# Performance work log

Hardware: AMD Instinct MI355X
Metric: run time of the kernel (lower is better)

Reference implementation:

```python
import jax, jax.numpy as jnp
import numpy as np

B = 4             # graphs per batch
POS_RANGE = 240.0 # pos lives in [0, 240)^3
VOXELS = (20.0, 30.0, 50.0, 80.0)
NEG = -1e30


def _basis(u):
    # open B-spline basis, degree 1, kernel_size 2, dim 3 -> 8 weights per edge
    cols = []
    for k in range(8):
        w = (u[:, 0] if k & 4 else 1.0 - u[:, 0])
        w = w * (u[:, 1] if k & 2 else 1.0 - u[:, 1])
        w = w * (u[:, 2] if k & 1 else 1.0 - u[:, 2])
        cols.append(w)
    return jnp.stack(cols, axis=1)  # [E, 8]


def _cartesian(pos, src, dst, emask):
    # T.Cartesian(cat=False, norm=True): rel pos scaled into [0,1]
    rel = pos[src] - pos[dst]
    m = jnp.max(jnp.where(emask[:, None], jnp.abs(rel), 0.0))
    return rel / (2.0 * jnp.maximum(m, 1e-9)) + 0.5


def _spline_conv(x, src, dst, pseudo, emask, W, Wr, b, n_nodes):
    # out_i = mean_{j->i} sum_k B_k(u_ij) x_j W_k + x_i Wr + b
    basis = _basis(pseudo) * emask[:, None].astype(x.dtype)  # [E,8]
    xk = jnp.einsum('ni,kio->nko', x, W)                     # [N,8,O]
    msg = basis[:, 0, None] * xk[src, 0]
    for k in range(1, 8):
        msg = msg + basis[:, k, None] * xk[src, k]           # [E,O]
    agg = jax.ops.segment_sum(msg, dst, num_segments=n_nodes)
    deg = jax.ops.segment_sum(emask.astype(x.dtype), dst, num_segments=n_nodes)
    return agg / jnp.maximum(deg, 1.0)[:, None] + x @ Wr + b


def _voxel_ids(pos, batch, vs):
    G = int(np.ceil(POS_RANGE / vs))
    c = jnp.clip(jnp.floor(pos / vs).astype(jnp.int64), 0, G - 1)
    cell = (c[:, 0] * G + c[:, 1]) * G + c[:, 2]
    return batch * (G ** 3) + cell, G ** 3


def _max_pool(x, pos, batch, valid, src, dst, emask, vs):
    # voxel-grid max pooling: nodes become fixed voxel cells (empty cells masked)
    nid, ncells = _voxel_ids(pos, batch, vs)
    n_new = B * ncells
    xm = jnp.where(valid[:, None], x, NEG)
    x_p = jax.ops.segment_max(xm, nid, num_segments=n_new)
    cnt = jax.ops.segment_sum(valid.astype(x.dtype), nid, num_segments=n_new)
    v_new = cnt > 0
    x_p = jnp.where(v_new[:, None], x_p, 0.0)
    pos_p = jax.ops.segment_sum(pos * valid[:, None].astype(pos.dtype), nid, num_segments=n_new)
    pos_p = pos_p / jnp.maximum(cnt, 1.0)[:, None]
    batch_p = jnp.arange(n_new, dtype=jnp.int64) // ncells
    # coarsen edges: remap to cells, drop self loops, coalesce at fixed size
    s2, d2 = nid[src], nid[dst]
    sent = n_new * n_new
    key = jnp.where(emask & (s2 != d2), s2 * n_new + d2, sent)
    uk = jnp.unique(key, size=key.shape[0], fill_value=sent)
    em = uk != sent
    uk = jnp.where(em, uk, 0)
    return x_p, pos_p, batch_p, v_new, uk // n_new, uk % n_new, em


def setup_inputs():
    key = jax.random.key(0)
    ks = jax.random.split(key, 24)
    NP, DEG = 5000, 8
    N = B * NP
    E = N * DEG
    x = jax.random.normal(ks[0], (N, 1), dtype=jnp.float32)
    pos = jax.random.uniform(ks[1], (N, 3), dtype=jnp.float32) * POS_RANGE
    src = jnp.repeat(jnp.arange(N, dtype=jnp.int64), DEG)
    delta = jax.random.randint(ks[2], (E,), 1, 100, dtype=jnp.int64)
    dst = (src // NP) * NP + (src % NP + delta) % NP   # intra-graph edges
    edge_index = jnp.stack([src, dst])
    batch = jnp.arange(N, dtype=jnp.int64) // NP
    sizes = [1, 64, 128, 256, 512]
    params = {}
    for l in range(4):
        ci, co = sizes[l], sizes[l + 1]
        params[f'W{l+1}'] = jax.random.normal(ks[3 + 3 * l], (8, ci, co), dtype=jnp.float32) / np.sqrt(8.0 * ci)
        params[f'Wr{l+1}'] = jax.random.normal(ks[4 + 3 * l], (ci, co), dtype=jnp.float32) / np.sqrt(float(ci))
        params[f'b{l+1}'] = jnp.zeros((co,), dtype=jnp.float32)
    params['fc1_w'] = jax.random.normal(ks[16], (64 * 512, 1024), dtype=jnp.float32) / np.sqrt(64.0 * 512.0)
    params['fc1_b'] = jnp.zeros((1024,), dtype=jnp.float32)
    params['fc2_w'] = jax.random.normal(ks[17], (1024, 1), dtype=jnp.float32) / np.sqrt(1024.0)
    params['fc2_b'] = jnp.zeros((1,), dtype=jnp.float32)
    return dict(x=x, pos=pos, edge_index=edge_index, batch=batch, **params)


def reference(x, pos, edge_index, batch, W1, Wr1, b1, W2, Wr2, b2, W3, Wr3, b3,
              W4, Wr4, b4, fc1_w, fc1_b, fc2_w, fc2_b):
    src, dst = edge_index[0], edge_index[1]
    n_nodes = x.shape[0]
    valid = jnp.ones((n_nodes,), dtype=bool)
    emask = jnp.ones((src.shape[0],), dtype=bool)
    Ws = [(W1, Wr1, b1), (W2, Wr2, b2), (W3, Wr3, b3), (W4, Wr4, b4)]
    for l in range(4):
        pseudo = _cartesian(pos, src, dst, emask)
        W, Wr, b = Ws[l]
        x = jax.nn.elu(_spline_conv(x, src, dst, pseudo, emask, W, Wr, b, n_nodes))
        if l < 3:
            x, pos, batch, valid, src, dst, emask = _max_pool(x, pos, batch, valid, src, dst, emask, VOXELS[l])
            n_nodes = x.shape[0]
    # MaxPoolingX(voxel=80, size=64): ceil(240/80)^3 = 27 <= 64 slots per graph
    nid, ncells = _voxel_ids(pos, batch, VOXELS[3])
    cluster = batch * 64 + (nid % ncells)
    xm = jnp.where(valid[:, None], x, NEG)
    xg = jax.ops.segment_max(xm, cluster, num_segments=B * 64)
    xg = jnp.where(xg <= NEG / 2, 0.0, xg)      # empty slots -> 0 (scatter-max default)
    xg = xg.reshape(B, 64 * 512)
    h = jax.nn.elu(xg @ fc1_w + fc1_b)           # dropout = identity (eval mode)
    return jax.nn.elu(h @ fc2_w + fc2_b)         # [B, 1]
```

## Files before the change

kernel.cpp:

```cpp
#include <hip/hip_runtime.h>

static constexpr int E0 = 160000;
static constexpr int NL0 = 20000;
static constexpr int NL1 = 6912;
static constexpr int NL2 = 2048;
static constexpr int NL3 = 500;

typedef short bf16x8 __attribute__((ext_vector_type(8)));
typedef float f32x4 __attribute__((ext_vector_type(4)));

__device__ __forceinline__ unsigned f2ord(float f) {
  unsigned u = __float_as_uint(f);
  return (u & 0x80000000u) ? ~u : (u | 0x80000000u);
}
__device__ __forceinline__ float ord2f(unsigned u) {
  unsigned v = (u & 0x80000000u) ? (u & 0x7fffffffu) : ~u;
  return __uint_as_float(v);
}
__device__ __forceinline__ float eluf(float x) { return x > 0.f ? x : expm1f(x); }
__device__ __forceinline__ void basis8(float u0, float u1, float u2, float* w) {
  float a0 = 1.f - u0, a1 = 1.f - u1, a2 = 1.f - u2;
  w[0] = a0*a1*a2; w[1] = a0*a1*u2; w[2] = a0*u1*a2; w[3] = a0*u1*u2;
  w[4] = u0*a1*a2; w[5] = u0*a1*u2; w[6] = u0*u1*a2; w[7] = u0*u1*u2;
}
__device__ __forceinline__ unsigned short f2b(float f) {
  unsigned u = __float_as_uint(f);
  return (unsigned short)((u + 0x7fffu + ((u >> 16) & 1u)) >> 16);
}
__device__ __forceinline__ float b2f(unsigned short h) {
  return __uint_as_float(((unsigned)h) << 16);
}
__device__ __forceinline__ int clampi(int v, int lo, int hi) {
  return v < lo ? lo : (v > hi ? hi : v);
}

__device__ __forceinline__ void mfma_tile(const unsigned short* __restrict__ Ah,
    const unsigned short* __restrict__ Al, const unsigned short* __restrict__ Bh,
    const unsigned short* __restrict__ Bl, int M, long K, int m0, int n0,
    int kbeg, int ksl, char* smem, f32x4* acc) {
  auto Ash = (unsigned short (*)[40])(smem);
  auto Asl = (unsigned short (*)[40])(smem + 5120);
  auto Bsh = (unsigned short (*)[40])(smem + 10240);
  auto Bsl = (unsigned short (*)[40])(smem + 15360);
  int t = threadIdx.x;
  int r = t >> 2, sg = (t & 3) * 8;
  int w = t >> 6, lane = t & 63;
  int ar = (w << 4) + (lane & 15), kq = (lane >> 4) << 3;
  for (int kt = 0; kt < ksl; kt += 32) {
    bf16x8 va = {}, vl = {};
    if (m0 + r < M) {
      long ga = (long)(m0 + r) * K + kbeg + kt + sg;
      va = *(const bf16x8*)&Ah[ga];
      vl = *(const bf16x8*)&Al[ga];
    }
    *(bf16x8*)&Ash[r][sg] = va;
    *(bf16x8*)&Asl[r][sg] = vl;
    long gb = (long)(n0 + r) * K + kbeg + kt + sg;
    *(bf16x8*)&Bsh[r][sg] = *(const bf16x8*)&Bh[gb];
    *(bf16x8*)&Bsl[r][sg] = *(const bf16x8*)&Bl[gb];
    __syncthreads();
    bf16x8 ah = *(const bf16x8*)&Ash[ar][kq];
    bf16x8 al = *(const bf16x8*)&Asl[ar][kq];
    #pragma unroll
    for (int nt = 0; nt < 4; nt++) {
      int br = (nt << 4) + (lane & 15);
      bf16x8 bh = *(const bf16x8*)&Bsh[br][kq];
      bf16x8 bl = *(const bf16x8*)&Bsl[br][kq];
      acc[nt] = __builtin_amdgcn_mfma_f32_16x16x32_bf16(al, bh, acc[nt], 0, 0, 0);
      acc[nt] = __builtin_amdgcn_mfma_f32_16x16x32_bf16(ah, bl, acc[nt], 0, 0, 0);
      acc[nt] = __builtin_amdgcn_mfma_f32_16x16x32_bf16(ah, bh, acc[nt], 0, 0, 0);
    }
    __syncthreads();
  }
}

__global__ __launch_bounds__(256)
void k_prep(const int* __restrict__ src0, const int* __restrict__ dst0,
            const float* __restrict__ pos0, const float* __restrict__ x0,
            int* __restrict__ degi, int4* __restrict__ erec0u, float* __restrict__ mbuf,
            const float* __restrict__ W1, const float* __restrict__ Wr1, float* __restrict__ wc1,
            const float* __restrict__ W2, const float* __restrict__ Wr2,
            const float* __restrict__ W3, const float* __restrict__ Wr3,
            const float* __restrict__ W4, const float* __restrict__ Wr4,
            unsigned short* __restrict__ w2h, unsigned short* __restrict__ w2l,
            unsigned short* __restrict__ w3h, unsigned short* __restrict__ w3l,
            unsigned short* __restrict__ w4h, unsigned short* __restrict__ w4l) {
  __shared__ __align__(16) float T[64][65];
  __shared__ float red[4];
  int tid = blockIdx.x * 256 + threadIdx.x, gsz = gridDim.x * 256;
  float v = 0.f;
  for (int e = tid; e < E0; e += gsz) {
    int s = src0[e], d = dst0[e];
    atomicAdd(&degi[d], 1);
    float r0 = pos0[s*3]   - pos0[d*3];
    float r1 = pos0[s*3+1] - pos0[d*3+1];
    float r2 = pos0[s*3+2] - pos0[d*3+2];
    erec0u[e] = make_int4(__float_as_int(x0[s]), __float_as_int(r0),
                          __float_as_int(r1), __float_as_int(r2));
    v = fmaxf(v, fmaxf(fabsf(r0), fmaxf(fabsf(r1), fabsf(r2))));
  }
  #pragma unroll
  for (int off = 32; off; off >>= 1) v = fmaxf(v, __shfl_down(v, off, 64));
  if ((threadIdx.x & 63) == 0) red[threadIdx.x >> 6] = v;
  __syncthreads();
  if (threadIdx.x == 0)
    atomicMax((unsigned*)mbuf,
              __float_as_uint(fmaxf(fmaxf(red[0], red[1]), fmaxf(red[2], red[3]))));
  for (int b = blockIdx.x; b < 378; b += gridDim.x) {
    const float *W, *Wr; unsigned short *oh, *ol; int K, N, kt, nt;
    if (b < 18)      { W = W2; Wr = Wr2; oh = w2h; ol = w2l; K = 576;  N = 128; kt = b / 2; nt = b % 2; }
    else if (b < 90) { int q = b - 18; W = W3; Wr = Wr3; oh = w3h; ol = w3l; K = 1152; N = 256; kt = q / 4; nt = q % 4; }
    else             { int q = b - 90; W = W4; Wr = Wr4; oh = w4h; ol = w4l; K = 2304; N = 512; kt = q / 8; nt = q % 8; }
    int k0 = kt * 64, n0 = nt * 64, KW = K - K / 9;
    __syncthreads();
    for (int i = threadIdx.x; i < 4096; i += 256) {
      int kk = i >> 6, nn = i & 63, k = k0 + kk;
      T[kk][nn] = (k < KW) ? W[(long)k * N + n0 + nn] : Wr[(long)(k - KW) * N + n0 + nn];
    }
    __syncthreads();
    for (int i = threadIdx.x; i < 4096; i += 256) {
      int nn = i >> 6, kk = i & 63;
      float vv = T[kk][nn];
      unsigned short hu = f2b(vv), lu = f2b(vv - b2f(hu));
      long o = (long)(n0 + nn) * K + k0 + kk;
      oh[o] = hu; ol[o] = lu;
    }
  }
  if (blockIdx.x == 0)
    for (int i = threadIdx.x; i < 576; i += 256)
      wc1[i] = (i < 512) ? W1[i] : Wr1[i - 512];
}

__global__ void k_alloc(int* __restrict__ degi, int* __restrict__ rowbeg,
                        int* __restrict__ rowlen, int* __restrict__ cursor,
                        int* __restrict__ ctr, int N) {
  int n = blockIdx.x * 256 + threadIdx.x;
  if (n >= N) return;
  int len = degi[n];
  int st = atomicAdd(ctr, len);
  rowbeg[n] = st; cursor[n] = st; rowlen[n] = len; degi[n] = 0;
}

__global__ void k_scat(const int4* __restrict__ eu, const int* __restrict__ du,
                       const int* __restrict__ ecnt, int ecap,
                       int* __restrict__ cursor, int4* __restrict__ es) {
  int n = ecnt ? *ecnt : ecap;
  for (int e = blockIdx.x * 256 + threadIdx.x; e < n; e += gridDim.x * 256) {
    int p = atomicAdd(&cursor[du[e]], 1);
    es[p] = eu[e];
  }
}

__global__ __launch_bounds__(256)
void k_l1(const float* __restrict__ pos0, const float* __restrict__ x0,
          const int4* __restrict__ erec, const int* __restrict__ rowbeg,
          const int* __restrict__ rowlen, const float* __restrict__ mbuf,
          const float* __restrict__ wc1, const float* __restrict__ b1,
          unsigned* __restrict__ pord1, float* __restrict__ cnt1,
          float* __restrict__ possum1, int* __restrict__ nid) {
  __shared__ float ys9[256][12];
  int t = threadIdx.x;
  int d = blockIdx.x * 256 + t;
  float inv = 0.5f / fmaxf(mbuf[0], 1e-9f);
  if (d < NL0) {
    int beg = rowbeg[d], len = rowlen[d];
    float acc[8] = {};
    for (int j = beg; j < beg + len; j++) {
      int4 rc = erec[j];
      float xv = __int_as_float(rc.x);
      float u0 = __int_as_float(rc.y) * inv + 0.5f;
      float u1 = __int_as_float(rc.z) * inv + 0.5f;
      float u2 = __int_as_float(rc.w) * inv + 0.5f;
      float w[8]; basis8(u0, u1, u2, w);
      #pragma unroll
      for (int k = 0; k < 8; k++) acc[k] += w[k] * xv;
    }
    float sc = 1.f / fmaxf((float)len, 1.f);
    #pragma unroll
    for (int k = 0; k < 8; k++) ys9[t][k] = acc[k] * sc;
    ys9[t][8]  = x0[d];
    ys9[t][9]  = pos0[d*3];
    ys9[t][10] = pos0[d*3+1];
    ys9[t][11] = pos0[d*3+2];
  }
  __syncthreads();
  int lane = t & 63, wv = t >> 6;
  float wcol[9];
  #pragma unroll
  for (int k = 0; k < 8; k++) wcol[k] = wc1[k * 64 + lane];
  wcol[8] = wc1[512 + lane];
  float bb = b1[lane];
  int base = blockIdx.x * 256 + wv * 64;
  for (int i = 0; i < 64; i++) {
    int dd = base + i;
    if (dd >= NL0) break;
    int li = wv * 64 + i;
    float v = bb + ys9[li][8] * wcol[8];
    #pragma unroll
    for (int k = 0; k < 8; k++) v += ys9[li][k] * wcol[k];
    v = eluf(v);
    float pd0 = ys9[li][9], pd1 = ys9[li][10], pd2 = ys9[li][11];
    int c0 = clampi((int)floorf(pd0 / 20.f), 0, 11);
    int c1 = clampi((int)floorf(pd1 / 20.f), 0, 11);
    int c2 = clampi((int)floorf(pd2 / 20.f), 0, 11);
    int id = (dd / 5000) * 1728 + (c0 * 12 + c1) * 12 + c2;
    atomicMax(&pord1[(long)id * 64 + lane], f2ord(v));
    if (lane == 0) {
      nid[dd] = id;
      atomicAdd(&cnt1[id], 1.f);
      atomicAdd(&possum1[id*3],   pd0);
      atomicAdd(&possum1[id*3+1], pd1);
      atomicAdd(&possum1[id*3+2], pd2);
    }
  }
}

__global__ __launch_bounds__(256)
void k_pedge(const int4* __restrict__ erecf, const int* __restrict__ srcf,
             const int* __restrict__ dstf, const int* __restrict__ ecntf, int ecap,
             const int* __restrict__ nid, int Nn, unsigned* __restrict__ bitmap,
             int4* __restrict__ erecu, int* __restrict__ dstu, int* __restrict__ ecntc,
             int* __restrict__ degi, const float* __restrict__ possum,
             const float* __restrict__ cnt, float* __restrict__ mo) {
  __shared__ float red[4];
  int n = ecntf ? *ecntf : ecap;
  int lane = threadIdx.x & 63;
  int stride = gridDim.x * 256;
  float vmax = 0.f;
  for (int base = blockIdx.x * 256; base < n; base += stride) {
    int e = base + threadIdx.x;
    bool win = false;
    int s2 = 0, d2 = 0;
    float r0 = 0.f, r1 = 0.f, r2 = 0.f;
    if (e < n) {
      int sL = erecf ? erecf[e].x : srcf[e];
      int dL = dstf[e];
      s2 = nid[sL]; d2 = nid[dL];
      if (s2 != d2) {
        float ics = 1.f / fmaxf(cnt[s2], 1.f), icd = 1.f / fmaxf(cnt[d2], 1.f);
        r0 = possum[s2*3]   * ics - possum[d2*3]   * icd;
        r1 = possum[s2*3+1] * ics - possum[d2*3+1] * icd;
        r2 = possum[s2*3+2] * ics - possum[d2*3+2] * icd;
        vmax = fmaxf(vmax, fmaxf(fabsf(r0), fmaxf(fabsf(r1), fabsf(r2))));
        unsigned key = (unsigned)s2 * (unsigned)Nn + (unsigned)d2;
        unsigned bit = 1u << (key & 31);
        unsigned old = atomicOr(&bitmap[key >> 5], bit);
        win = !(old & bit);
      }
    }
    unsigned long long mask = __ballot(win);
    if (mask) {
      int leader = __ffsll((unsigned long long)mask) - 1;
      int bq = 0;
      if (lane == leader) bq = atomicAdd(ecntc, __popcll(mask));
      bq = __shfl(bq, leader, 64);
      if (win) {
        int q = bq + __popcll(mask & ((1ULL << lane) - 1ULL));
        erecu[q] = make_int4(s2, __float_as_int(r0), __float_as_int(r1), __float_as_int(r2));
        dstu[q] = d2;
        atomicAdd(&degi[d2], 1);
      }
    }
  }
  #pragma unroll
  for (int off = 32; off; off >>= 1) vmax = fmaxf(vmax, __shfl_down(vmax, off, 64));
  if ((threadIdx.x & 63) == 0) red[threadIdx.x >> 6] = vmax;
  __syncthreads();
  if (threadIdx.x == 0)
    atomicMax((unsigned*)mo,
              __float_as_uint(fmaxf(fmaxf(red[0], red[1]), fmaxf(red[2], red[3]))));
}

template<int ES>
__global__ __launch_bounds__(256)
void k_gather(const unsigned* __restrict__ pordc, const int4* __restrict__ erec,
              const int* __restrict__ rowbeg, const int* __restrict__ rowlen,
              const float* __restrict__ mbuf,
              unsigned short* __restrict__ ysh, unsigned short* __restrict__ ysl,
              int N, int Ci, int nchunk) {
  __shared__ float comb[4][64][8];
  int wv = threadIdx.x >> 6, lane = threadIdx.x & 63;
  int gw = blockIdx.x * 4 + wv;
  int job = gw / ES, sub = gw % ES;
  int d = job / nchunk, ch = job % nchunk;
  bool active = d < N;
  float inv = 0.5f / fmaxf(mbuf[0], 1e-9f);
  int co = ch * 64 + lane;
  float acc[8] = {};
  int beg = 0, len = 0;
  if (active) {
    beg = rowbeg[d]; len = rowlen[d];
    int end = beg + len;
    int j = beg + sub;
    for (; j + 3 * ES < end; j += 4 * ES) {
      int4 ra = erec[j], rb = erec[j + ES], rc = erec[j + 2 * ES], rd = erec[j + 3 * ES];
      float xa = ord2f(pordc[(long)ra.x * Ci + co]);
      float xb = ord2f(pordc[(long)rb.x * Ci + co]);
      float xc = ord2f(pordc[(long)rc.x * Ci + co]);
      float xd = ord2f(pordc[(long)rd.x * Ci + co]);
      float wa[8], wb[8], wc[8], wd[8];
      basis8(__int_as_float(ra.y) * inv + 0.5f, __int_as_float(ra.z) * inv + 0.5f,
             __int_as_float(ra.w) * inv + 0.5f, wa);
      basis8(__int_as_float(rb.y) * inv + 0.5f, __int_as_float(rb.z) * inv + 0.5f,
             __int_as_float(rb.w) * inv + 0.5f, wb);
      basis8(__int_as_float(rc.y) * inv + 0.5f, __int_as_float(rc.z) * inv + 0.5f,
             __int_as_float(rc.w) * inv + 0.5f, wc);
      basis8(__int_as_float(rd.y) * inv + 0.5f, __int_as_float(rd.z) * inv + 0.5f,
             __int_as_float(rd.w) * inv + 0.5f, wd);
      #pragma unroll
      for (int k = 0; k < 8; k++)
        acc[k] += wa[k] * xa + wb[k] * xb + wc[k] * xc + wd[k] * xd;
    }
    for (; j < end; j += ES) {
      int4 ra = erec[j];
      float xa = ord2f(pordc[(long)ra.x * Ci + co]);
      float wa[8];
      basis8(__int_as_float(ra.y) * inv + 0.5f, __int_as_float(ra.z) * inv + 0.5f,
             __int_as_float(ra.w) * inv + 0.5f, wa);
      #pragma unroll
      for (int k = 0; k < 8; k++) acc[k] += wa[k] * xa;
    }
  }
  if (ES > 1) {
    #pragma unroll
    for (int k = 0; k < 8; k++) comb[wv][lane][k] = acc[k];
    __syncthreads();
    if (sub != 0 || !active) return;
    #pragma unroll
    for (int s = 1; s < ES; s++)
      #pragma unroll
      for (int k = 0; k < 8; k++) acc[k] += comb[wv + s][lane][k];
  } else if (!active) return;
  float sc = 1.f / fmaxf((float)len, 1.f);
  long row = (long)d * 9 * Ci;
  #pragma unroll
  for (int k = 0; k < 8; k++) {
    float v = acc[k] * sc;
    unsigned short hu = f2b(v);
    ysh[row + k * Ci + co] = hu;
    ysl[row + k * Ci + co] = f2b(v - b2f(hu));
  }
  unsigned od = pordc[(long)d * Ci + co];
  float xdv = (od == 0u) ? 0.f : ord2f(od);
  unsigned short hu = f2b(xdv);
  ysh[row + 8 * Ci + co] = hu;
  ysl[row + 8 * Ci + co] = f2b(xdv - b2f(hu));
}

__global__ __launch_bounds__(256)
void k_gemmpool(const unsigned short* __restrict__ ysh, const unsigned short* __restrict__ ysl,
                const unsigned short* __restrict__ Bh, const unsigned short* __restrict__ Bl,
                int M, int N, int K, const float* __restrict__ bias,
                const float* __restrict__ possum, const float* __restrict__ cnt,
                int div, float vs, int G, int NC,
                unsigned* __restrict__ pordn, float* __restrict__ cntn,
                float* __restrict__ possumn, int* __restrict__ nid) {
  __shared__ __align__(16) char smem[20480];
  int nbx = N >> 6;
  int bx = blockIdx.x % nbx, by = blockIdx.x / nbx;
  int m0 = by * 64, n0 = bx * 64;
  f32x4 acc[4] = {};
  mfma_tile(ysh, ysl, Bh, Bl, M, K, m0, n0, 0, K, smem, acc);
  int w = threadIdx.x >> 6, lane = threadIdx.x & 63;
  int row0 = m0 + (w << 4) + ((lane >> 4) << 2);
  int colb = n0 + (lane & 15);
  #pragma unroll
  for (int q = 0; q < 4; q++) {
    int gm = row0 + q;
    float c = cnt[gm];
    float ic = 1.f / fmaxf(c, 1.f);
    float p0 = possum[gm*3] * ic, p1 = possum[gm*3+1] * ic, p2 = possum[gm*3+2] * ic;
    int c0 = clampi((int)floorf(p0 / vs), 0, G - 1);
    int c1 = clampi((int)floorf(p1 / vs), 0, G - 1);
    int c2 = clampi((int)floorf(p2 / vs), 0, G - 1);
    int id = (gm / div) * NC + (c0 * G + c1) * G + c2;
    bool vl = c > 0.f;
    if (bx == 0 && (lane & 15) == 0) {
      nid[gm] = id;
      if (vl) {
        atomicAdd(&cntn[id], 1.f);
        atomicAdd(&possumn[id*3],   p0);
        atomicAdd(&possumn[id*3+1], p1);
        atomicAdd(&possumn[id*3+2], p2);
      }
    }
    if (vl) {
      #pragma unroll
      for (int nt = 0; nt < 4; nt++) {
        int col = colb + nt * 16;
        float v = eluf(acc[nt][q] + bias[col]);
        atomicMax(&pordn[(long)id * N + col], f2ord(v));
      }
    }
  }
}

__global__ __launch_bounds__(256)
void k_gemm4(const unsigned short* __restrict__ ysh, const unsigned short* __restrict__ ysl,
             const unsigned short* __restrict__ Bh, const unsigned short* __restrict__ Bl,
             float* __restrict__ Cp) {
  __shared__ __align__(16) char smem[20480];
  int z = blockIdx.x >> 6, rem = blockIdx.x & 63, bx = rem & 7, by = rem >> 3;
  int m0 = by * 64, n0 = bx * 64;
  f32x4 acc[4] = {};
  mfma_tile(ysh, ysl, Bh, Bl, 500, 2304, m0, n0, z * 576, 576, smem, acc);
  float* Co = Cp + (long)z * 256000;
  int w = threadIdx.x >> 6, lane = threadIdx.x & 63;
  int row0 = m0 + (w << 4) + ((lane >> 4) << 2);
  int colb = n0 + (lane & 15);
  #pragma unroll
  for (int nt = 0; nt < 4; nt++)
    #pragma unroll
    for (int q = 0; q < 4; q++) {
      int gm = row0 + q;
      if (gm < 500) Co[(long)gm * 512 + colb + nt * 16] = acc[nt][q];
    }
}

__global__ void k_reduce4(const float* __restrict__ Cp, const float* __restrict__ b4,
                          const float* __restrict__ possum3, const float* __restrict__ cnt3,
                          unsigned* __restrict__ xg) {
  int idx = blockIdx.x * 256 + threadIdx.x;
  if (idx >= 256000) return;
  int n = idx >> 9, o = idx & 511;
  float s = Cp[idx] + Cp[idx + 256000] + Cp[idx + 512000] + Cp[idx + 768000];
  float v = eluf(s + b4[o]);
  float c = cnt3[n];
  if (c <= 0.f) return;
  float ic = 1.f / c;
  float p0 = possum3[n*3] * ic, p1 = possum3[n*3+1] * ic, p2 = possum3[n*3+2] * ic;
  int c0 = clampi((int)floorf(p0 / 80.f), 0, 2);
  int c1 = clampi((int)floorf(p1 / 80.f), 0, 2);
  int c2 = clampi((int)floorf(p2 / 80.f), 0, 2);
  int cl = (n / 125) * 64 + (c0 * 3 + c1) * 3 + c2;
  atomicMax(&xg[(long)cl * 512 + o], f2ord(v));
}

__global__ __launch_bounds__(128)
void k_fc1(const unsigned* __restrict__ xg_ord, const float* __restrict__ w,
           float* __restrict__ h) {
  int cellhalf = blockIdx.x >> 3, jb = blockIdx.x & 7;
  int cell = cellhalf >> 1, half = cellhalf & 1;
  int j = jb * 128 + threadIdx.x;
  __shared__ float xs[4][256];
  for (int q = threadIdx.x; q < 1024; q += 128) {
    int b = q >> 8, ci = q & 255;
    unsigned o = xg_ord[((b * 64 + cell) << 9) + half * 256 + ci];
    xs[b][ci] = (o == 0u) ? 0.f : ord2f(o);
  }
  __syncthreads();
  float a0 = 0, a1 = 0, a2 = 0, a3 = 0;
  int cbase = cell * 512 + half * 256;
  for (int ci = 0; ci < 256; ci++) {
    float ww = w[(long)(cbase + ci) * 1024 + j];
    a0 += xs[0][ci] * ww; a1 += xs[1][ci] * ww;
    a2 += xs[2][ci] * ww; a3 += xs[3][ci] * ww;
  }
  atomicAdd(&h[j], a0);        atomicAdd(&h[1024 + j], a1);
  atomicAdd(&h[2048 + j], a2); atomicAdd(&h[3072 + j], a3);
}

__global__ void k_fc2(const float* __restrict__ h, const float* __restrict__ fb1,
                      const float* __restrict__ w, const float* __restrict__ b,
                      float* __restrict__ out) {
  int bb = blockIdx.x, t = threadIdx.x;
  float a = 0;
  for (int j = t; j < 1024; j += 256) a += eluf(h[bb * 1024 + j] + fb1[j]) * w[j];
  for (int off = 32; off; off >>= 1) a += __shfl_down(a, off, 64);
  __shared__ float red[4];
  int lane = t & 63, wv = t >> 6;
  if (lane == 0) red[wv] = a;
  __syncthreads();
  if (t == 0) out[bb] = eluf(red[0] + red[1] + red[2] + red[3] + b[0]);
}

extern "C" void kernel_launch(void* const* d_in, const int* in_sizes, int n_in,
                              void* d_out, int out_size, void* d_ws, size_t ws_size,
                              hipStream_t stream) {
  const float* x0   = (const float*)d_in[0];
  const float* pos0 = (const float*)d_in[1];
  const int*   ei   = (const int*)d_in[2];
  const float* W1 = (const float*)d_in[4],  *Wr1 = (const float*)d_in[5],  *b1 = (const float*)d_in[6];
  const float* W2 = (const float*)d_in[7],  *Wr2 = (const float*)d_in[8],  *b2 = (const float*)d_in[9];
  const float* W3 = (const float*)d_in[10], *Wr3 = (const float*)d_in[11], *b3 = (const float*)d_in[12];
  const float* W4 = (const float*)d_in[13], *Wr4 = (const float*)d_in[14], *b4 = (const float*)d_in[15];
  const float* fw1 = (const float*)d_in[16], *fb1 = (const float*)d_in[17];
  const float* fw2 = (const float*)d_in[18], *fb2 = (const float*)d_in[19];
  float* out = (float*)d_out;
  const int* src0 = ei;
  const int* dst0 = ei + E0;

  char* ws = (char*)d_ws;
  size_t off = 0;
  auto alloc = [&](size_t bytes) -> void* {
    off = (off + 255) & ~(size_t)255;
    void* q = ws + off; off += bytes; return q;
  };
  int4* erec0u = (int4*)alloc((size_t)E0 * 16);
  int4* erec_s = (int4*)alloc((size_t)E0 * 16);
  int4* eu_a   = (int4*)alloc((size_t)E0 * 16);
  int4* eu_b   = (int4*)alloc((size_t)E0 * 16);
  int* du_a = (int*)alloc(E0 * 4);
  int* du_b = (int*)alloc(E0 * 4);
  int* nid  = (int*)alloc(NL0 * 4);
  int* rowbeg = (int*)alloc(NL0 * 4);
  int* rowlen = (int*)alloc(NL0 * 4);
  int* cursor = (int*)alloc(NL0 * 4);
  unsigned short* ysh = (unsigned short*)alloc((size_t)NL1 * 576 * 2);
  unsigned short* ysl = (unsigned short*)alloc((size_t)NL1 * 576 * 2);
  float* wc1 = (float*)alloc(576 * 4);
  unsigned short* w2h = (unsigned short*)alloc((size_t)576 * 128 * 2);
  unsigned short* w2l = (unsigned short*)alloc((size_t)576 * 128 * 2);
  unsigned short* w3h = (unsigned short*)alloc((size_t)1152 * 256 * 2);
  unsigned short* w3l = (unsigned short*)alloc((size_t)1152 * 256 * 2);
  unsigned short* w4h = (unsigned short*)alloc((size_t)2304 * 512 * 2);
  unsigned short* w4l = (unsigned short*)alloc((size_t)2304 * 512 * 2);
  float* Cp = (float*)alloc((size_t)4 * 256000 * 4);
  char* z0 = (char*)alloc(0);
  unsigned* pord1 = (unsigned*)alloc((size_t)NL1 * 64 * 4);
  unsigned* pord2 = (unsigned*)alloc((size_t)NL2 * 128 * 4);
  unsigned* pord3 = (unsigned*)alloc((size_t)NL3 * 256 * 4);
  unsigned* xg    = (unsigned*)alloc((size_t)4 * 64 * 512 * 4);
  float* cnt1 = (float*)alloc(NL1 * 4);
  float* cnt2 = (float*)alloc(NL2 * 4);
  float* cnt3 = (float*)alloc(NL3 * 4);
  float* possum1 = (float*)alloc(NL1 * 12);
  float* possum2 = (float*)alloc(NL2 * 12);
  float* possum3 = (float*)alloc(NL3 * 12);
  size_t bm1w = ((size_t)NL1 * NL1 + 31) / 32;
  size_t bm2w = ((size_t)NL2 * NL2 + 31) / 32;
  size_t bm3w = ((size_t)NL3 * NL3 + 31) / 32;
  unsigned* bm1 = (unsigned*)alloc(bm1w * 4);
  unsigned* bm2 = (unsigned*)alloc(bm2w * 4);
  unsigned* bm3 = (unsigned*)alloc(bm3w * 4);
  int* degi = (int*)alloc(NL0 * 4);
  float* mbuf = (float*)alloc(64);
  int* ecnt = (int*)(mbuf + 8);
  int* ctr  = (int*)(mbuf + 12);
  float* h = (float*)alloc(4096 * 4);
  char* zend = (char*)alloc(0);
  size_t zbytes = (size_t)(zend - z0);
  (void)ws_size; (void)in_sizes; (void)n_in; (void)out_size;

  auto cdiv = [](long a, long b) { return (int)((a + b - 1) / b); };

  hipMemsetAsync(z0, 0, zbytes, stream);

  k_prep<<<512, 256, 0, stream>>>(src0, dst0, pos0, x0, degi, erec0u, mbuf,
                                  W1, Wr1, wc1, W2, Wr2, W3, Wr3, W4, Wr4,
                                  w2h, w2l, w3h, w3l, w4h, w4l);
  k_alloc<<<cdiv(NL0, 256), 256, 0, stream>>>(degi, rowbeg, rowlen, cursor, ctr + 0, NL0);
  k_scat<<<512, 256, 0, stream>>>(erec0u, dst0, nullptr, E0, cursor, erec_s);
  k_l1<<<cdiv(NL0, 256), 256, 0, stream>>>(pos0, x0, erec_s, rowbeg, rowlen, mbuf,
                                           wc1, b1, pord1, cnt1, possum1, nid);
  k_pedge<<<512, 256, 0, stream>>>(nullptr, src0, dst0, nullptr, E0, nid, NL1, bm1,
                                   eu_a, du_a, ecnt + 0, degi, possum1, cnt1, mbuf + 1);
  k_alloc<<<cdiv(NL1, 256), 256, 0, stream>>>(degi, rowbeg, rowlen, cursor, ctr + 1, NL1);
  k_scat<<<512, 256, 0, stream>>>(eu_a, du_a, ecnt + 0, E0, cursor, erec_s);
  k_gather<1><<<cdiv(NL1, 4), 256, 0, stream>>>(pord1, erec_s, rowbeg, rowlen, mbuf + 1,
                                                ysh, ysl, NL1, 64, 1);
  k_gemmpool<<<(128 / 64) * (NL1 / 64), 256, 0, stream>>>(
      ysh, ysl, w2h, w2l, NL1, 128, 576, b2, possum1, cnt1,
      1728, 30.f, 8, 512, pord2, cnt2, possum2, nid);
  k_pedge<<<512, 256, 0, stream>>>(eu_a, nullptr, du_a, ecnt + 0, E0, nid, NL2, bm2,
                                   eu_b, du_b, ecnt + 1, degi, possum2, cnt2, mbuf + 2);
  k_alloc<<<cdiv(NL2, 256), 256, 0, stream>>>(degi, rowbeg, rowlen, cursor, ctr + 2, NL2);
  k_scat<<<512, 256, 0, stream>>>(eu_b, du_b, ecnt + 1, E0, cursor, erec_s);
  k_gather<2><<<cdiv(NL2 * 2 * 2, 4), 256, 0, stream>>>(pord2, erec_s, rowbeg, rowlen, mbuf + 2,
                                                        ysh, ysl, NL2, 128, 2);
  k_gemmpool<<<(256 / 64) * (NL2 / 64), 256, 0, stream>>>(
      ysh, ysl, w3h, w3l, NL2, 256, 1152, b3, possum2, cnt2,
      512, 50.f, 5, 125, pord3, cnt3, possum3, nid);
  k_pedge<<<512, 256, 0, stream>>>(eu_b, nullptr, du_b, ecnt + 1, E0, nid, NL3, bm3,
                                   eu_a, du_a, ecnt + 2, degi, possum3, cnt3, mbuf + 3);
  k_alloc<<<cdiv(NL3, 256), 256, 0, stream>>>(degi, rowbeg, rowlen, cursor, ctr + 3, NL3);
  k_scat<<<512, 256, 0, stream>>>(eu_a, du_a, ecnt + 2, E0, cursor, erec_s);
  k_gather<4><<<cdiv(NL3 * 4 * 4, 4), 256, 0, stream>>>(pord3, erec_s, rowbeg, rowlen, mbuf + 3,
                                                        ysh, ysl, NL3, 256, 4);
  k_gemm4<<<256, 256, 0, stream>>>(ysh, ysl, w4h, w4l, Cp);
  k_reduce4<<<cdiv(256000, 256), 256, 0, stream>>>(Cp, b4, possum3, cnt3, xg);
  k_fc1<<<27 * 2 * 8, 128, 0, stream>>>(xg, fw1, h);
  k_fc2<<<4, 256, 0, stream>>>(h, fb1, fw2, fb2, out);
}
```

Before: 413.1 us.

## Split layer-1 conv into edge-parallel aggregation and per-node pooling kernels

The fused layer-1 kernel is split in two. The first kernel assigns 8 threads per destination node to walk its edge list, reduces the 8 basis accumulators with xor shuffles, and writes them to a global scratch buffer. The second kernel gives each node its own wavefront to do the small matvec, ELU and voxel atomics. Before, one thread walked each node's whole edge list and one wave serially looped over 64 nodes for the pooling atomics, so the goal is more parallelism and less serial latency. The cost is an extra launch and a global round trip through the scratch buffer.

```diff
diff --git a/kernel.cpp b/kernel.cpp
--- a/kernel.cpp
+++ b/kernel.cpp
@@ -152,66 +152,69 @@
 }
 
 __global__ __launch_bounds__(256)
-void k_l1(const float* __restrict__ pos0, const float* __restrict__ x0,
-          const int4* __restrict__ erec, const int* __restrict__ rowbeg,
-          const int* __restrict__ rowlen, const float* __restrict__ mbuf,
-          const float* __restrict__ wc1, const float* __restrict__ b1,
-          unsigned* __restrict__ pord1, float* __restrict__ cnt1,
-          float* __restrict__ possum1, int* __restrict__ nid) {
-  __shared__ float ys9[256][12];
+void k_l1a(const int4* __restrict__ erec, const int* __restrict__ rowbeg,
+           const int* __restrict__ rowlen, const float* __restrict__ mbuf,
+           float* __restrict__ ysg) {
   int t = threadIdx.x;
-  int d = blockIdx.x * 256 + t;
+  int d = blockIdx.x * 32 + (t >> 3);
+  if (d >= NL0) return;
+  int sub = t & 7;
   float inv = 0.5f / fmaxf(mbuf[0], 1e-9f);
-  if (d < NL0) {
-    int beg = rowbeg[d], len = rowlen[d];
-    float acc[8] = {};
-    for (int j = beg; j < beg + len; j++) {
-      int4 rc = erec[j];
-      float xv = __int_as_float(rc.x);
-      float u0 = __int_as_float(rc.y) * inv + 0.5f;
-      float u1 = __int_as_float(rc.z) * inv + 0.5f;
-      float u2 = __int_as_float(rc.w) * inv + 0.5f;
-      float w[8]; basis8(u0, u1, u2, w);
-      #pragma unroll
-      for (int k = 0; k < 8; k++) acc[k] += w[k] * xv;
-    }
+  int beg = rowbeg[d], len = rowlen[d], end = beg + len;
+  float acc[8] = {};
+  for (int j = beg + sub; j < end; j += 8) {
+    int4 rc = erec[j];
+    float xv = __int_as_float(rc.x);
+    float w[8];
+    basis8(__int_as_float(rc.y) * inv + 0.5f, __int_as_float(rc.z) * inv + 0.5f,
+           __int_as_float(rc.w) * inv + 0.5f, w);
+    #pragma unroll
+    for (int k = 0; k < 8; k++) acc[k] += w[k] * xv;
+  }
+  #pragma unroll
+  for (int m = 1; m < 8; m <<= 1)
+    #pragma unroll
+    for (int k = 0; k < 8; k++) acc[k] += __shfl_xor(acc[k], m, 64);
+  if (sub == 0) {
     float sc = 1.f / fmaxf((float)len, 1.f);
-    #pragma unroll
-    for (int k = 0; k < 8; k++) ys9[t][k] = acc[k] * sc;
-    ys9[t][8]  = x0[d];
-    ys9[t][9]  = pos0[d*3];
-    ys9[t][10] = pos0[d*3+1];
-    ys9[t][11] = pos0[d*3+2];
-  }
-  __syncthreads();
-  int lane = t & 63, wv = t >> 6;
+    float4 o0 = make_float4(acc[0]*sc, acc[1]*sc, acc[2]*sc, acc[3]*sc);
+    float4 o1 = make_float4(acc[4]*sc, acc[5]*sc, acc[6]*sc, acc[7]*sc);
+    *(float4*)&ysg[d*8]     = o0;
+    *(float4*)&ysg[d*8 + 4] = o1;
+  }
+}
+
+__global__ __launch_bounds__(256)
+void k_l1b(const float* __restrict__ ysg, const float* __restrict__ x0,
+           const float* __restrict__ pos0, const float* __restrict__ wc1,
+           const float* __restrict__ b1,
+           unsigned* __restrict__ pord1, float* __restrict__ cnt1,
+           float* __restrict__ possum1, int* __restrict__ nid) {
+  int wv = threadIdx.x >> 6, lane = threadIdx.x & 63;
+  int d = blockIdx.x * 4 + wv;
+  if (d >= NL0) return;
   float wcol[9];
   #pragma unroll
   for (int k = 0; k < 8; k++) wcol[k] = wc1[k * 64 + lane];
   wcol[8] = wc1[512 + lane];
-  float bb = b1[lane];
-  int base = blockIdx.x * 256 + wv * 64;
-  for (int i = 0; i < 64; i++) {
-    int dd = base + i;
-    if (dd >= NL0) break;
-    int li = wv * 64 + i;
-    float v = bb + ys9[li][8] * wcol[8];
-    #pragma unroll
-    for (int k = 0; k < 8; k++) v += ys9[li][k] * wcol[k];
-    v = eluf(v);
-    float pd0 = ys9[li][9], pd1 = ys9[li][10], pd2 = ys9[li][11];
-    int c0 = clampi((int)floorf(pd0 / 20.f), 0, 11);
-    int c1 = clampi((int)floorf(pd1 / 20.f), 0, 11);
-    int c2 = clampi((int)floorf(pd2 / 20.f), 0, 11);
-    int id = (dd / 5000) * 1728 + (c0 * 12 + c1) * 12 + c2;
-    atomicMax(&pord1[(long)id * 64 + lane], f2ord(v));
-    if (lane == 0) {
-      nid[dd] = id;
-      atomicAdd(&cnt1[id], 1.f);
-      atomicAdd(&possum1[id*3],   pd0);
-      atomicAdd(&possum1[id*3+1], pd1);
-      atomicAdd(&possum1[id*3+2], pd2);
-    }
+  float4 a0 = *(const float4*)&ysg[d*8];
+  float4 a1 = *(const float4*)&ysg[d*8 + 4];
+  float v = b1[lane] + x0[d] * wcol[8]
+          + a0.x * wcol[0] + a0.y * wcol[1] + a0.z * wcol[2] + a0.w * wcol[3]
+          + a1.x * wcol[4] + a1.y * wcol[5] + a1.z * wcol[6] + a1.w * wcol[7];
+  v = eluf(v);
+  float pd0 = pos0[d*3], pd1 = pos0[d*3+1], pd2 = pos0[d*3+2];
+  int c0 = clampi((int)floorf(pd0 / 20.f), 0, 11);
+  int c1 = clampi((int)floorf(pd1 / 20.f), 0, 11);
+  int c2 = clampi((int)floorf(pd2 / 20.f), 0, 11);
+  int id = (d / 5000) * 1728 + (c0 * 12 + c1) * 12 + c2;
+  atomicMax(&pord1[(long)id * 64 + lane], f2ord(v));
+  if (lane == 0) {
+    nid[d] = id;
+    atomicAdd(&cnt1[id], 1.f);
+    atomicAdd(&possum1[id*3],   pd0);
+    atomicAdd(&possum1[id*3+1], pd1);
+    atomicAdd(&possum1[id*3+2], pd2);
   }
 }
 
@@ -506,6 +509,7 @@
   int* rowbeg = (int*)alloc(NL0 * 4);
   int* rowlen = (int*)alloc(NL0 * 4);
   int* cursor = (int*)alloc(NL0 * 4);
+  float* ysg = (float*)alloc((size_t)NL0 * 8 * 4);
   unsigned short* ysh = (unsigned short*)alloc((size_t)NL1 * 576 * 2);
   unsigned short* ysl = (unsigned short*)alloc((size_t)NL1 * 576 * 2);
   float* wc1 = (float*)alloc(576 * 4);
@@ -551,8 +555,8 @@
                                   w2h, w2l, w3h, w3l, w4h, w4l);
   k_alloc<<<cdiv(NL0, 256), 256, 0, stream>>>(degi, rowbeg, rowlen, cursor, ctr + 0, NL0);
   k_scat<<<512, 256, 0, stream>>>(erec0u, dst0, nullptr, E0, cursor, erec_s);
-  k_l1<<<cdiv(NL0, 256), 256, 0, stream>>>(pos0, x0, erec_s, rowbeg, rowlen, mbuf,
-                                           wc1, b1, pord1, cnt1, possum1, nid);
+  k_l1a<<<cdiv(NL0, 32), 256, 0, stream>>>(erec_s, rowbeg, rowlen, mbuf, ysg);
+  k_l1b<<<cdiv(NL0, 4), 256, 0, stream>>>(ysg, x0, pos0, wc1, b1, pord1, cnt1, possum1, nid);
   k_pedge<<<512, 256, 0, stream>>>(nullptr, src0, dst0, nullptr, E0, nid, NL1, bm1,
                                    eu_a, du_a, ecnt + 0, degi, possum1, cnt1, mbuf + 1);
   k_alloc<<<cdiv(NL1, 256), 256, 0, stream>>>(degi, rowbeg, rowlen, cursor, ctr + 1, NL1);
```

New measurement: 412.2 us, median of 2. Within noise of the previous version (-0.2%).
